# Kernel tuning notes

Hardware: AMD Instinct MI355X
Metric: run time of the kernel (lower is better)

## Reference

```python
import jax, jax.numpy as jnp
import numpy as np

N = 8192
E = 262144
IN_DIM = 512
H1 = 256
H2 = 64


def setup_inputs() -> dict:
    key = jax.random.key(0)
    ks = jax.random.split(key, 12)
    stdv1 = 1.0 / np.sqrt(H1)
    stdv2 = 1.0 / np.sqrt(H2)
    return {
        "edge_row": jax.random.randint(ks[0], (E,), 0, N),
        "edge_col": jax.random.randint(ks[1], (E,), 0, N),
        "edge_val": jax.random.uniform(ks[2], (E,), dtype=jnp.float32),
        "features": jax.random.normal(ks[3], (N, IN_DIM), dtype=jnp.float32),
        "W1": jax.random.uniform(ks[4], (IN_DIM, H1), minval=-stdv1, maxval=stdv1, dtype=jnp.float32),
        "b1": jax.random.uniform(ks[5], (H1,), minval=-stdv1, maxval=stdv1, dtype=jnp.float32),
        "W2": jax.random.uniform(ks[6], (H1, H2), minval=-stdv2, maxval=stdv2, dtype=jnp.float32),
        "b2": jax.random.uniform(ks[7], (H2,), minval=-stdv2, maxval=stdv2, dtype=jnp.float32),
        "W3": jax.random.uniform(ks[8], (H1, H2), minval=-stdv2, maxval=stdv2, dtype=jnp.float32),
        "b3": jax.random.uniform(ks[9], (H2,), minval=-stdv2, maxval=stdv2, dtype=jnp.float32),
        "noise": jax.random.normal(ks[10], (N, H2), dtype=jnp.float32),
    }


def _gcn(edge_row, edge_col, edge_val, x, W, b):
    # support = X @ W ; out = A_hat @ support (sparse COO spmm) ; tanh(out + b)
    support = x @ W                                   # [N, out]
    msg = edge_val[:, None] * support[edge_col]       # [E, out]
    out = jax.ops.segment_sum(msg, edge_row, num_segments=N)
    return jnp.tanh(out + b)


def reference(edge_row, edge_col, edge_val, features, W1, b1, W2, b2, W3, b3, noise):
    h = _gcn(edge_row, edge_col, edge_val, features, W1, b1)   # [N, H1]
    mean = _gcn(edge_row, edge_col, edge_val, h, W2, b2)       # [N, H2]
    log_std = _gcn(edge_row, edge_col, edge_val, h, W3, b3)    # [N, H2]
    z = mean + noise * jnp.exp(log_std)                        # reparameterization
    adj_rec = jax.nn.sigmoid(z @ z.T)                          # [N, N]
    return adj_rec, z
```

## Files before the change

kernel.cpp:

```cpp
#include <hip/hip_runtime.h>
#include <math.h>

static constexpr int NN  = 8192;
static constexpr int EE  = 262144;
static constexpr int IND = 512;
static constexpr int HH1 = 256;
static constexpr int RCAP = 128;

typedef _Float16 f16x8  __attribute__((ext_vector_type(8)));
typedef _Float16 f16x4  __attribute__((ext_vector_type(4)));
typedef _Float16 f16x2  __attribute__((ext_vector_type(2)));
typedef float    f32x4  __attribute__((ext_vector_type(4)));

static __device__ __forceinline__ float fast_sigmoid(float x) {
    float e = __expf(-x);
    return __builtin_amdgcn_rcpf(1.f + e);
}

__global__ __launch_bounds__(256) void k_prepw_scatter(const float* __restrict__ W1,
                                                       const float* __restrict__ W2,
                                                       const float* __restrict__ W3,
                                                       _Float16* __restrict__ W1T,
                                                       _Float16* __restrict__ W23T,
                                                       const int* __restrict__ erow,
                                                       const int* __restrict__ ecol,
                                                       const float* __restrict__ eval,
                                                       int* __restrict__ cnt,
                                                       int2* __restrict__ epack) {
    int b = blockIdx.x;
    if (b >= 160) {
        int e = (b - 160) * 256 + threadIdx.x;
        int r = erow[e];
        int pos = atomicAdd(&cnt[r], 1);
        epack[(size_t)r * RCAP + pos] = make_int2(ecol[e], __float_as_int(eval[e]));
        return;
    }
    __shared__ float tile[32][33];
    int c = threadIdx.x & 31;
    int r0 = threadIdx.x >> 5;
    if (b < 128) {
        int tk = b >> 3;
        int tn = b & 7;
#pragma unroll
        for (int i = 0; i < 4; i++) {
            int r = r0 * 4 + i;
            tile[r][c] = W1[(tk * 32 + r) * HH1 + tn * 32 + c];
        }
        __syncthreads();
#pragma unroll
        for (int i = 0; i < 4; i++) {
            int rr = r0 * 4 + i;
            W1T[(tn * 32 + rr) * IND + tk * 32 + c] = (_Float16)tile[c][rr];
        }
    } else {
        int t = b - 128;
        int tk = t >> 2;
        int tn = t & 3;
        const float* Wsrc = (tn < 2) ? W2 : W3;
        int nc0 = (tn & 1) * 32;
#pragma unroll
        for (int i = 0; i < 4; i++) {
            int r = r0 * 4 + i;
            tile[r][c] = Wsrc[(tk * 32 + r) * 64 + nc0 + c];
        }
        __syncthreads();
#pragma unroll
        for (int i = 0; i < 4; i++) {
            int rr = r0 * 4 + i;
            W23T[(tn * 32 + rr) * HH1 + tk * 32 + c] = (_Float16)tile[c][rr];
        }
    }
}

__global__ __launch_bounds__(256) void k_gemm1_mfma(const float* __restrict__ X,
                                                    const _Float16* __restrict__ B,
                                                    _Float16* __restrict__ out) {
    int b = blockIdx.x;
    int bm = b >> 1, bn = b & 1;
    int w = threadIdx.x >> 6, l = threadIdx.x & 63;
    int wm = w >> 1, wn = w & 1;
    int lr = l & 15, kg = l >> 4;
    int row0 = bm * 32 + wm * 16;
    int col0 = bn * 128 + wn * 64;

    f32x4 acc[4];
#pragma unroll
    for (int nt = 0; nt < 4; nt++) acc[nt] = (f32x4){0.f, 0.f, 0.f, 0.f};

    for (int ks = 0; ks < IND; ks += 32) {
        int ko = ks + kg * 8;
        const float* xp = &X[(size_t)(row0 + lr) * IND + ko];
        float4 x0 = *(const float4*)xp;
        float4 x1 = *(const float4*)(xp + 4);
        f16x8 a = {(_Float16)x0.x, (_Float16)x0.y, (_Float16)x0.z, (_Float16)x0.w,
                   (_Float16)x1.x, (_Float16)x1.y, (_Float16)x1.z, (_Float16)x1.w};
        f16x8 bb[4];
#pragma unroll
        for (int nt = 0; nt < 4; nt++)
            bb[nt] = *(const f16x8*)&B[(size_t)(col0 + nt * 16 + lr) * IND + ko];
#pragma unroll
        for (int nt = 0; nt < 4; nt++)
            acc[nt] = __builtin_amdgcn_mfma_f32_16x16x32_f16(a, bb[nt], acc[nt], 0, 0, 0);
    }
#pragma unroll
    for (int nt = 0; nt < 4; nt++)
#pragma unroll
        for (int r = 0; r < 4; r++)
            out[(size_t)(row0 + kg * 4 + r) * HH1 + col0 + nt * 16 + lr] = (_Float16)acc[nt][r];
}

__global__ __launch_bounds__(256) void k_spmm1v(const int* __restrict__ cnt,
                                                const int2* __restrict__ epack,
                                                const _Float16* __restrict__ sup,
                                                const float* __restrict__ b1,
                                                _Float16* __restrict__ hb) {
    int w = threadIdx.x >> 6, l = threadIdx.x & 63;
    int row = blockIdx.x * 4 + w;
    int s = row * RCAP, eend = s + cnt[row];
    float4 acc = make_float4(0.f, 0.f, 0.f, 0.f);
    int i = s;
    for (; i + 4 <= eend; i += 4) {
        int2 p0 = epack[i];
        int2 p1 = epack[i + 1];
        int2 p2 = epack[i + 2];
        int2 p3 = epack[i + 3];
        f16x4 t0 = *(const f16x4*)&sup[(size_t)p0.x * HH1 + l * 4];
        f16x4 t1 = *(const f16x4*)&sup[(size_t)p1.x * HH1 + l * 4];
        f16x4 t2 = *(const f16x4*)&sup[(size_t)p2.x * HH1 + l * 4];
        f16x4 t3 = *(const f16x4*)&sup[(size_t)p3.x * HH1 + l * 4];
        float v0 = __int_as_float(p0.y), v1 = __int_as_float(p1.y);
        float v2 = __int_as_float(p2.y), v3 = __int_as_float(p3.y);
        acc.x += v0 * (float)t0[0] + v1 * (float)t1[0] + v2 * (float)t2[0] + v3 * (float)t3[0];
        acc.y += v0 * (float)t0[1] + v1 * (float)t1[1] + v2 * (float)t2[1] + v3 * (float)t3[1];
        acc.z += v0 * (float)t0[2] + v1 * (float)t1[2] + v2 * (float)t2[2] + v3 * (float)t3[2];
        acc.w += v0 * (float)t0[3] + v1 * (float)t1[3] + v2 * (float)t2[3] + v3 * (float)t3[3];
    }
    for (; i < eend; i++) {
        int2 p0 = epack[i];
        f16x4 t0 = *(const f16x4*)&sup[(size_t)p0.x * HH1 + l * 4];
        float v0 = __int_as_float(p0.y);
        acc.x += v0 * (float)t0[0];
        acc.y += v0 * (float)t0[1];
        acc.z += v0 * (float)t0[2];
        acc.w += v0 * (float)t0[3];
    }
    float4 bb = ((const float4*)b1)[l];
    f16x4 o;
    o[0] = (_Float16)tanhf(acc.x + bb.x);
    o[1] = (_Float16)tanhf(acc.y + bb.y);
    o[2] = (_Float16)tanhf(acc.z + bb.z);
    o[3] = (_Float16)tanhf(acc.w + bb.w);
    *(f16x4*)&hb[(size_t)row * HH1 + l * 4] = o;
}

__global__ __launch_bounds__(256) void k_gemm23_mfma(const _Float16* __restrict__ A,
                                                     const _Float16* __restrict__ B,
                                                     _Float16* __restrict__ out) {
    int bm = blockIdx.x;
    int w = threadIdx.x >> 6, l = threadIdx.x & 63;
    int lr = l & 15, kg = l >> 4;
    int row0 = bm * 16;
    int col0 = w * 32;

    f32x4 acc[2];
#pragma unroll
    for (int nt = 0; nt < 2; nt++) acc[nt] = (f32x4){0.f, 0.f, 0.f, 0.f};

    for (int ks = 0; ks < HH1; ks += 32) {
        int ko = ks + kg * 8;
        f16x8 a = *(const f16x8*)&A[(size_t)(row0 + lr) * HH1 + ko];
        f16x8 bb[2];
#pragma unroll
        for (int nt = 0; nt < 2; nt++)
            bb[nt] = *(const f16x8*)&B[(size_t)(col0 + nt * 16 + lr) * HH1 + ko];
#pragma unroll
        for (int nt = 0; nt < 2; nt++)
            acc[nt] = __builtin_amdgcn_mfma_f32_16x16x32_f16(a, bb[nt], acc[nt], 0, 0, 0);
    }
#pragma unroll
    for (int nt = 0; nt < 2; nt++)
#pragma unroll
        for (int r = 0; r < 4; r++)
            out[(size_t)(row0 + kg * 4 + r) * 128 + col0 + nt * 16 + lr] = (_Float16)acc[nt][r];
}

__global__ __launch_bounds__(256) void k_spmm23v(const int* __restrict__ cnt,
                                                 const int2* __restrict__ epack,
                                                 const _Float16* __restrict__ s23,
                                                 const float* __restrict__ b2,
                                                 const float* __restrict__ b3,
                                                 const float* __restrict__ noise,
                                                 float* __restrict__ zout,
                                                 _Float16* __restrict__ zh) {
    int w = threadIdx.x >> 6, l = threadIdx.x & 63;
    int row = blockIdx.x * 4 + w;
    int s = row * RCAP, eend = s + cnt[row];
    float ax = 0.f, ay = 0.f;
    int i = s;
    for (; i + 4 <= eend; i += 4) {
        int2 p0 = epack[i];
        int2 p1 = epack[i + 1];
        int2 p2 = epack[i + 2];
        int2 p3 = epack[i + 3];
        f16x2 t0 = *(const f16x2*)&s23[(size_t)p0.x * 128 + l * 2];
        f16x2 t1 = *(const f16x2*)&s23[(size_t)p1.x * 128 + l * 2];
        f16x2 t2 = *(const f16x2*)&s23[(size_t)p2.x * 128 + l * 2];
        f16x2 t3 = *(const f16x2*)&s23[(size_t)p3.x * 128 + l * 2];
        float v0 = __int_as_float(p0.y), v1 = __int_as_float(p1.y);
        float v2 = __int_as_float(p2.y), v3 = __int_as_float(p3.y);
        ax += v0 * (float)t0[0] + v1 * (float)t1[0] + v2 * (float)t2[0] + v3 * (float)t3[0];
        ay += v0 * (float)t0[1] + v1 * (float)t1[1] + v2 * (float)t2[1] + v3 * (float)t3[1];
    }
    for (; i < eend; i++) {
        int2 p0 = epack[i];
        f16x2 t0 = *(const f16x2*)&s23[(size_t)p0.x * 128 + l * 2];
        float v0 = __int_as_float(p0.y);
        ax += v0 * (float)t0[0];
        ay += v0 * (float)t0[1];
    }
    float bx, by;
    if (l < 32) { bx = b2[2 * l]; by = b2[2 * l + 1]; }
    else        { bx = b3[2 * (l - 32)]; by = b3[2 * (l - 32) + 1]; }
    float t0 = tanhf(ax + bx);
    float t1 = tanhf(ay + by);
    float u0 = __shfl_xor(t0, 32, 64);
    float u1 = __shfl_xor(t1, 32, 64);
    if (l < 32) {
        float2 nz = ((const float2*)noise)[(size_t)row * 32 + l];
        float z0 = t0 + nz.x * __expf(u0);
        float z1 = t1 + nz.y * __expf(u1);
        ((float2*)zout)[(size_t)row * 32 + l] = make_float2(z0, z1);
        *(f16x2*)&zh[(size_t)row * 64 + l * 2] = (f16x2){(_Float16)z0, (_Float16)z1};
    }
}

__global__ __launch_bounds__(256) void k_zzt_mfma(const _Float16* __restrict__ zh,
                                                  float* __restrict__ adj) {
    int bi = blockIdx.y, bj = blockIdx.x;
    int tid = threadIdx.x;
    int w = tid >> 6, l = tid & 63;
    int lr = l & 15, kg = l >> 4;
    const int i0 = bi * 128 + w * 32;
    const int j0 = bj * 128;

    f16x8 a[2][2];
#pragma unroll
    for (int mt = 0; mt < 2; mt++)
#pragma unroll
        for (int kk = 0; kk < 2; kk++)
            a[mt][kk] = *(const f16x8*)&zh[(size_t)(i0 + mt * 16 + lr) * 64 + kk * 32 + kg * 8];

    f32x4 acc[2][8];
#pragma unroll
    for (int mt = 0; mt < 2; mt++)
#pragma unroll
        for (int nt = 0; nt < 8; nt++)
            acc[mt][nt] = (f32x4){0.f, 0.f, 0.f, 0.f};

#pragma unroll
    for (int nt = 0; nt < 8; nt++) {
        f16x8 b0 = *(const f16x8*)&zh[(size_t)(j0 + nt * 16 + lr) * 64 + 0  + kg * 8];
        f16x8 b1 = *(const f16x8*)&zh[(size_t)(j0 + nt * 16 + lr) * 64 + 32 + kg * 8];
        acc[0][nt] = __builtin_amdgcn_mfma_f32_16x16x32_f16(a[0][0], b0, acc[0][nt], 0, 0, 0);
        acc[0][nt] = __builtin_amdgcn_mfma_f32_16x16x32_f16(a[0][1], b1, acc[0][nt], 0, 0, 0);
        acc[1][nt] = __builtin_amdgcn_mfma_f32_16x16x32_f16(a[1][0], b0, acc[1][nt], 0, 0, 0);
        acc[1][nt] = __builtin_amdgcn_mfma_f32_16x16x32_f16(a[1][1], b1, acc[1][nt], 0, 0, 0);
    }

#pragma unroll
    for (int nt = 0; nt < 8; nt++) {
#pragma unroll
        for (int mt = 0; mt < 2; mt++) {
            size_t orow = (size_t)(j0 + nt * 16 + lr);
            size_t ocol = (size_t)(i0 + mt * 16 + kg * 4);
            float4 o;
            o.x = fast_sigmoid(acc[mt][nt][0]);
            o.y = fast_sigmoid(acc[mt][nt][1]);
            o.z = fast_sigmoid(acc[mt][nt][2]);
            o.w = fast_sigmoid(acc[mt][nt][3]);
            *(float4*)&adj[orow * NN + ocol] = o;
        }
    }
}

extern "C" void kernel_launch(void* const* d_in, const int* in_sizes, int n_in,
                              void* d_out, int out_size, void* d_ws, size_t ws_size,
                              hipStream_t stream) {
    const int*   erow  = (const int*)d_in[0];
    const int*   ecol  = (const int*)d_in[1];
    const float* eval  = (const float*)d_in[2];
    const float* X     = (const float*)d_in[3];
    const float* W1    = (const float*)d_in[4];
    const float* b1    = (const float*)d_in[5];
    const float* W2    = (const float*)d_in[6];
    const float* b2    = (const float*)d_in[7];
    const float* W3    = (const float*)d_in[8];
    const float* b3    = (const float*)d_in[9];
    const float* noise = (const float*)d_in[10];

    float* adj  = (float*)d_out;
    float* zout = (float*)d_out + (size_t)NN * NN;

    char* ws = (char*)d_ws;
    int*  cnt       = (int*)(ws + 0);
    int2* epack     = (int2*)(ws + 32768);
    _Float16* W1T   = (_Float16*)(ws + 8421376);
    _Float16* W23T  = (_Float16*)(ws + 8683520);
    _Float16* zh    = (_Float16*)(ws + 8749056);

    char* ob = (char*)d_out;
    _Float16* sup1h = (_Float16*)(ob + 0);
    _Float16* hb    = (_Float16*)(ob + 4194304);
    _Float16* s23h  = (_Float16*)(ob + 8388608);

    hipMemsetAsync(cnt, 0, NN * sizeof(int), stream);
    k_prepw_scatter<<<160 + EE / 256, 256, 0, stream>>>(W1, W2, W3, W1T, W23T,
                                                        erow, ecol, eval, cnt, epack);
    k_gemm1_mfma<<<512, 256, 0, stream>>>(X, W1T, sup1h);
    k_spmm1v<<<NN / 4, 256, 0, stream>>>(cnt, epack, sup1h, b1, hb);
    k_gemm23_mfma<<<512, 256, 0, stream>>>(hb, W23T, s23h);
    k_spmm23v<<<NN / 4, 256, 0, stream>>>(cnt, epack, s23h, b2, b3, noise, zout, zh);
    k_zzt_mfma<<<dim3(64, 64), 256, 0, stream>>>(zh, adj);
}
```

Measured before the change: 152.9 us.

## Fuse spmm1 with gemm23, merge edge scatter into gemm1, drop memset

Replaces the memset with a zeroing branch in a new init kernel that also transposes the weights. The edge scatter now runs as extra blocks of the first GEMM launch, so the two overlap. The first sparse aggregation is fused with the second GEMM: each 512-thread block builds 16 rows of h in shared memory and multiplies them by W23T with MFMA, so h never goes to global memory and two launches are removed. The cost is fewer warps in flight for the gather-heavy spmm phase and only one MFMA tile per wave in the fused GEMM.

Measured after the change: 142.1 us (median of 3 runs). -7.1%, faster.

```diff
diff --git a/kernel.cpp b/kernel.cpp
--- a/kernel.cpp
+++ b/kernel.cpp
@@ -17,65 +17,71 @@
     return __builtin_amdgcn_rcpf(1.f + e);
 }
 
-__global__ __launch_bounds__(256) void k_prepw_scatter(const float* __restrict__ W1,
-                                                       const float* __restrict__ W2,
-                                                       const float* __restrict__ W3,
-                                                       _Float16* __restrict__ W1T,
-                                                       _Float16* __restrict__ W23T,
+__global__ __launch_bounds__(256) void k_init(const float* __restrict__ W1,
+                                              const float* __restrict__ W2,
+                                              const float* __restrict__ W3,
+                                              _Float16* __restrict__ W1T,
+                                              _Float16* __restrict__ W23T,
+                                              int* __restrict__ cnt) {
+    int b = blockIdx.x;
+    if (b < 32) {
+        cnt[b * 256 + threadIdx.x] = 0;
+        return;
+    }
+    __shared__ float tile[32][33];
+    int c = threadIdx.x & 31;
+    int r0 = threadIdx.x >> 5;
+    if (b < 160) {
+        int t = b - 32;
+        int tk = t >> 3;
+        int tn = t & 7;
+#pragma unroll
+        for (int i = 0; i < 4; i++) {
+            int r = r0 * 4 + i;
+            tile[r][c] = W1[(tk * 32 + r) * HH1 + tn * 32 + c];
+        }
+        __syncthreads();
+#pragma unroll
+        for (int i = 0; i < 4; i++) {
+            int rr = r0 * 4 + i;
+            W1T[(tn * 32 + rr) * IND + tk * 32 + c] = (_Float16)tile[c][rr];
+        }
+    } else {
+        int t = b - 160;
+        int tk = t >> 2;
+        int tn = t & 3;
+        const float* Wsrc = (tn < 2) ? W2 : W3;
+        int nc0 = (tn & 1) * 32;
+#pragma unroll
+        for (int i = 0; i < 4; i++) {
+            int r = r0 * 4 + i;
+            tile[r][c] = Wsrc[(tk * 32 + r) * 64 + nc0 + c];
+        }
+        __syncthreads();
+#pragma unroll
+        for (int i = 0; i < 4; i++) {
+            int rr = r0 * 4 + i;
+            W23T[(tn * 32 + rr) * HH1 + tk * 32 + c] = (_Float16)tile[c][rr];
+        }
+    }
+}
+
+__global__ __launch_bounds__(256) void k_gemm1_scatter(const float* __restrict__ X,
+                                                       const _Float16* __restrict__ B,
+                                                       _Float16* __restrict__ out,
                                                        const int* __restrict__ erow,
                                                        const int* __restrict__ ecol,
                                                        const float* __restrict__ eval,
                                                        int* __restrict__ cnt,
                                                        int2* __restrict__ epack) {
     int b = blockIdx.x;
-    if (b >= 160) {
-        int e = (b - 160) * 256 + threadIdx.x;
+    if (b >= 512) {
+        int e = (b - 512) * 256 + threadIdx.x;
         int r = erow[e];
         int pos = atomicAdd(&cnt[r], 1);
         epack[(size_t)r * RCAP + pos] = make_int2(ecol[e], __float_as_int(eval[e]));
         return;
     }
-    __shared__ float tile[32][33];
-    int c = threadIdx.x & 31;
-    int r0 = threadIdx.x >> 5;
-    if (b < 128) {
-        int tk = b >> 3;
-        int tn = b & 7;
-#pragma unroll
-        for (int i = 0; i < 4; i++) {
-            int r = r0 * 4 + i;
-            tile[r][c] = W1[(tk * 32 + r) * HH1 + tn * 32 + c];
-        }
-        __syncthreads();
-#pragma unroll
-        for (int i = 0; i < 4; i++) {
-            int rr = r0 * 4 + i;
-            W1T[(tn * 32 + rr) * IND + tk * 32 + c] = (_Float16)tile[c][rr];
-        }
-    } else {
-        int t = b - 128;
-        int tk = t >> 2;
-        int tn = t & 3;
-        const float* Wsrc = (tn < 2) ? W2 : W3;
-        int nc0 = (tn & 1) * 32;
-#pragma unroll
-        for (int i = 0; i < 4; i++) {
-            int r = r0 * 4 + i;
-            tile[r][c] = Wsrc[(tk * 32 + r) * 64 + nc0 + c];
-        }
-        __syncthreads();
-#pragma unroll
-        for (int i = 0; i < 4; i++) {
-            int rr = r0 * 4 + i;
-            W23T[(tn * 32 + rr) * HH1 + tk * 32 + c] = (_Float16)tile[c][rr];
-        }
-    }
-}
-
-__global__ __launch_bounds__(256) void k_gemm1_mfma(const float* __restrict__ X,
-                                                    const _Float16* __restrict__ B,
-                                                    _Float16* __restrict__ out) {
-    int b = blockIdx.x;
     int bm = b >> 1, bn = b & 1;
     int w = threadIdx.x >> 6, l = threadIdx.x & 63;
     int wm = w >> 1, wn = w & 1;
@@ -109,79 +115,70 @@
             out[(size_t)(row0 + kg * 4 + r) * HH1 + col0 + nt * 16 + lr] = (_Float16)acc[nt][r];
 }
 
-__global__ __launch_bounds__(256) void k_spmm1v(const int* __restrict__ cnt,
-                                                const int2* __restrict__ epack,
-                                                const _Float16* __restrict__ sup,
-                                                const float* __restrict__ b1,
-                                                _Float16* __restrict__ hb) {
+__global__ __launch_bounds__(512) void k_spmm1_gemm23(const int* __restrict__ cnt,
+                                                      const int2* __restrict__ epack,
+                                                      const _Float16* __restrict__ sup,
+                                                      const float* __restrict__ b1,
+                                                      const _Float16* __restrict__ W23T,
+                                                      _Float16* __restrict__ s23h) {
+    __shared__ _Float16 hs[16][264];
     int w = threadIdx.x >> 6, l = threadIdx.x & 63;
-    int row = blockIdx.x * 4 + w;
-    int s = row * RCAP, eend = s + cnt[row];
-    float4 acc = make_float4(0.f, 0.f, 0.f, 0.f);
-    int i = s;
-    for (; i + 4 <= eend; i += 4) {
-        int2 p0 = epack[i];
-        int2 p1 = epack[i + 1];
-        int2 p2 = epack[i + 2];
-        int2 p3 = epack[i + 3];
-        f16x4 t0 = *(const f16x4*)&sup[(size_t)p0.x * HH1 + l * 4];
-        f16x4 t1 = *(const f16x4*)&sup[(size_t)p1.x * HH1 + l * 4];
-        f16x4 t2 = *(const f16x4*)&sup[(size_t)p2.x * HH1 + l * 4];
-        f16x4 t3 = *(const f16x4*)&sup[(size_t)p3.x * HH1 + l * 4];
-        float v0 = __int_as_float(p0.y), v1 = __int_as_float(p1.y);
-        float v2 = __int_as_float(p2.y), v3 = __int_as_float(p3.y);
-        acc.x += v0 * (float)t0[0] + v1 * (float)t1[0] + v2 * (float)t2[0] + v3 * (float)t3[0];
-        acc.y += v0 * (float)t0[1] + v1 * (float)t1[1] + v2 * (float)t2[1] + v3 * (float)t3[1];
-        acc.z += v0 * (float)t0[2] + v1 * (float)t1[2] + v2 * (float)t2[2] + v3 * (float)t3[2];
-        acc.w += v0 * (float)t0[3] + v1 * (float)t1[3] + v2 * (float)t2[3] + v3 * (float)t3[3];
-    }
-    for (; i < eend; i++) {
-        int2 p0 = epack[i];
-        f16x4 t0 = *(const f16x4*)&sup[(size_t)p0.x * HH1 + l * 4];
-        float v0 = __int_as_float(p0.y);
-        acc.x += v0 * (float)t0[0];
-        acc.y += v0 * (float)t0[1];
-        acc.z += v0 * (float)t0[2];
-        acc.w += v0 * (float)t0[3];
-    }
-    float4 bb = ((const float4*)b1)[l];
-    f16x4 o;
-    o[0] = (_Float16)tanhf(acc.x + bb.x);
-    o[1] = (_Float16)tanhf(acc.y + bb.y);
-    o[2] = (_Float16)tanhf(acc.z + bb.z);
-    o[3] = (_Float16)tanhf(acc.w + bb.w);
-    *(f16x4*)&hb[(size_t)row * HH1 + l * 4] = o;
-}
-
-__global__ __launch_bounds__(256) void k_gemm23_mfma(const _Float16* __restrict__ A,
-                                                     const _Float16* __restrict__ B,
-                                                     _Float16* __restrict__ out) {
-    int bm = blockIdx.x;
-    int w = threadIdx.x >> 6, l = threadIdx.x & 63;
+    int brow0 = blockIdx.x * 16;
+
+#pragma unroll
+    for (int rr = 0; rr < 2; rr++) {
+        int rloc = w * 2 + rr;
+        int row = brow0 + rloc;
+        int s = row * RCAP, eend = s + cnt[row];
+        float4 acc = make_float4(0.f, 0.f, 0.f, 0.f);
+        int i = s;
+        for (; i + 4 <= eend; i += 4) {
+            int2 p0 = epack[i];
+            int2 p1 = epack[i + 1];
+            int2 p2 = epack[i + 2];
+            int2 p3 = epack[i + 3];
+            f16x4 t0 = *(const f16x4*)&sup[(size_t)p0.x * HH1 + l * 4];
+            f16x4 t1 = *(const f16x4*)&sup[(size_t)p1.x * HH1 + l * 4];
+            f16x4 t2 = *(const f16x4*)&sup[(size_t)p2.x * HH1 + l * 4];
+            f16x4 t3 = *(const f16x4*)&sup[(size_t)p3.x * HH1 + l * 4];
+            float v0 = __int_as_float(p0.y), v1 = __int_as_float(p1.y);
+            float v2 = __int_as_float(p2.y), v3 = __int_as_float(p3.y);
+            acc.x += v0 * (float)t0[0] + v1 * (float)t1[0] + v2 * (float)t2[0] + v3 * (float)t3[0];
+            acc.y += v0 * (float)t0[1] + v1 * (float)t1[1] + v2 * (float)t2[1] + v3 * (float)t3[1];
+            acc.z += v0 * (float)t0[2] + v1 * (float)t1[2] + v2 * (float)t2[2] + v3 * (float)t3[2];
+            acc.w += v0 * (float)t0[3] + v1 * (float)t1[3] + v2 * (float)t2[3] + v3 * (float)t3[3];
+        }
+        for (; i < eend; i++) {
+            int2 p0 = epack[i];
+            f16x4 t0 = *(const f16x4*)&sup[(size_t)p0.x * HH1 + l * 4];
+            float v0 = __int_as_float(p0.y);
+            acc.x += v0 * (float)t0[0];
+            acc.y += v0 * (float)t0[1];
+            acc.z += v0 * (float)t0[2];
+            acc.w += v0 * (float)t0[3];
+        }
+        float4 bb = ((const float4*)b1)[l];
+        f16x4 o;
+        o[0] = (_Float16)tanhf(acc.x + bb.x);
+        o[1] = (_Float16)tanhf(acc.y + bb.y);
+        o[2] = (_Float16)tanhf(acc.z + bb.z);
+        o[3] = (_Float16)tanhf(acc.w + bb.w);
+        *(f16x4*)&hs[rloc][l * 4] = o;
+    }
+    __syncthreads();
+
     int lr = l & 15, kg = l >> 4;
-    int row0 = bm * 16;
-    int col0 = w * 32;
-
-    f32x4 acc[2];
-#pragma unroll
-    for (int nt = 0; nt < 2; nt++) acc[nt] = (f32x4){0.f, 0.f, 0.f, 0.f};
-
+    int colbase = w * 16;
+    f32x4 acc = (f32x4){0.f, 0.f, 0.f, 0.f};
     for (int ks = 0; ks < HH1; ks += 32) {
         int ko = ks + kg * 8;
-        f16x8 a = *(const f16x8*)&A[(size_t)(row0 + lr) * HH1 + ko];
-        f16x8 bb[2];
-#pragma unroll
-        for (int nt = 0; nt < 2; nt++)
-            bb[nt] = *(const f16x8*)&B[(size_t)(col0 + nt * 16 + lr) * HH1 + ko];
-#pragma unroll
-        for (int nt = 0; nt < 2; nt++)
-            acc[nt] = __builtin_amdgcn_mfma_f32_16x16x32_f16(a, bb[nt], acc[nt], 0, 0, 0);
-    }
-#pragma unroll
-    for (int nt = 0; nt < 2; nt++)
-#pragma unroll
-        for (int r = 0; r < 4; r++)
-            out[(size_t)(row0 + kg * 4 + r) * 128 + col0 + nt * 16 + lr] = (_Float16)acc[nt][r];
+        f16x8 a = *(const f16x8*)&hs[lr][ko];
+        f16x8 bfrag = *(const f16x8*)&W23T[(size_t)(colbase + lr) * HH1 + ko];
+        acc = __builtin_amdgcn_mfma_f32_16x16x32_f16(a, bfrag, acc, 0, 0, 0);
+    }
+#pragma unroll
+    for (int r = 0; r < 4; r++)
+        s23h[(size_t)(brow0 + kg * 4 + r) * 128 + colbase + lr] = (_Float16)acc[r];
 }
 
 __global__ __launch_bounds__(256) void k_spmm23v(const int* __restrict__ cnt,
@@ -310,15 +307,12 @@
 
     char* ob = (char*)d_out;
     _Float16* sup1h = (_Float16*)(ob + 0);
-    _Float16* hb    = (_Float16*)(ob + 4194304);
-    _Float16* s23h  = (_Float16*)(ob + 8388608);
-
-    hipMemsetAsync(cnt, 0, NN * sizeof(int), stream);
-    k_prepw_scatter<<<160 + EE / 256, 256, 0, stream>>>(W1, W2, W3, W1T, W23T,
+    _Float16* s23h  = (_Float16*)(ob + 4194304);
+
+    k_init<<<192, 256, 0, stream>>>(W1, W2, W3, W1T, W23T, cnt);
+    k_gemm1_scatter<<<512 + EE / 256, 256, 0, stream>>>(X, W1T, sup1h,
                                                         erow, ecol, eval, cnt, epack);
-    k_gemm1_mfma<<<512, 256, 0, stream>>>(X, W1T, sup1h);
-    k_spmm1v<<<NN / 4, 256, 0, stream>>>(cnt, epack, sup1h, b1, hb);
-    k_gemm23_mfma<<<512, 256, 0, stream>>>(hb, W23T, s23h);
+    k_spmm1_gemm23<<<512, 512, 0, stream>>>(cnt, epack, sup1h, b1, W23T, s23h);
     k_spmm23v<<<NN / 4, 256, 0, stream>>>(cnt, epack, s23h, b2, b3, noise, zout, zh);
     k_zzt_mfma<<<dim3(64, 64), 256, 0, stream>>>(zh, adj);
 }
```
